# Performance work log

Hardware: AMD Instinct MI355X
Metric: run time of the kernel (lower is better)

## Reference

```python
import jax, jax.numpy as jnp
import numpy as np
import math

NB_HEADS = 16
NUM_BUCKETS = 32
MAX_DISTANCE = 128


def _rel_bucket(qlen, klen, num_buckets=NUM_BUCKETS, max_distance=MAX_DISTANCE):
    # static (numpy) computation of T5 relative-position buckets, bidirectional
    relpos = np.arange(qlen)[:, None] - np.arange(klen)[None, :]
    n = -relpos
    nb = num_buckets // 2
    ret = (n < 0).astype(np.int64) * nb
    n = np.abs(n)
    max_exact = nb // 2
    is_small = n < max_exact
    val_if_large = max_exact + (
        np.log(np.maximum(n, 1) / max_exact) / math.log(max_distance / max_exact) * (nb - max_exact)
    ).astype(np.int64)
    val_if_large = np.minimum(val_if_large, nb - 1)
    return ret + np.where(is_small, n, val_if_large)


def _layer_normalize(x):
    # faithful to source: mean/biased-std over last dim, NO epsilon, no affine
    m = jnp.mean(x, axis=-1, keepdims=True)
    var = jnp.mean((x - m) ** 2, axis=-1, keepdims=True)
    return (x - m) / jnp.sqrt(var)


def setup_inputs() -> dict:
    key = jax.random.key(0)
    ks = jax.random.split(key, 16)
    B, L, D, F = 4, 1024, 1024, 4096
    s = 0.02
    inp = {
        "x": jax.random.normal(ks[0], (B, L, D), jnp.float32),
        "padding_mask": jnp.ones((B, L), jnp.int32),
        "Wq": jax.random.normal(ks[1], (D, D), jnp.float32) * s,
        "bq": jnp.zeros((D,), jnp.float32),
        "Wk": jax.random.normal(ks[2], (D, D), jnp.float32) * s,
        "bk": jnp.zeros((D,), jnp.float32),
        "Wv": jax.random.normal(ks[3], (D, D), jnp.float32) * s,
        "bv": jnp.zeros((D,), jnp.float32),
        "Wo": jax.random.normal(ks[4], (D, D), jnp.float32) * s,
        "bo": jnp.zeros((D,), jnp.float32),
        "rel_emb": jax.random.normal(ks[5], (NUM_BUCKETS, NB_HEADS), jnp.float32) * s,
        "W1": jax.random.normal(ks[6], (F, D), jnp.float32) * s,
        "b1": jnp.zeros((F,), jnp.float32),
        "W2": jax.random.normal(ks[7], (D, F), jnp.float32) * s,
        "b2": jnp.zeros((D,), jnp.float32),
    }
    return inp


def reference(x, padding_mask, Wq, bq, Wk, bk, Wv, bv, Wo, bo, rel_emb, W1, b1, W2, b2):
    B, L, D = x.shape
    H = NB_HEADS
    dh = D // H

    q = x @ Wq.T + bq
    k = x @ Wk.T + bk
    v = x @ Wv.T + bv

    # NOTE: source does a RAW reshape (B, L, H*dh) -> (B*H, L, dh); reproduce exactly
    qm = q.reshape(B * H, L, dh)
    km = k.reshape(B * H, L, dh)
    vm = v.reshape(B * H, L, dh)

    scores = jnp.einsum("bqd,bkd->bqk", qm, km)  # (B*H, L, L), no 1/sqrt(dh) scaling in source

    # relative position bias: emb[bucket] -> (L, L, H), tile heads B times, permute
    buckets = jnp.asarray(_rel_bucket(L, L))
    pos = rel_emb[buckets]                      # (L, L, H)
    bias = jnp.transpose(jnp.tile(pos, (1, 1, B)), (2, 0, 1))  # (H*B, L, L)
    scores = scores + bias

    # padding mask in log space, tiled exactly like source's repeat+view
    pm = jnp.log(padding_mask.astype(jnp.float32))            # (B, L)
    mask = jnp.tile(pm[:, None, :], (1, L, H)).reshape(-1, L, L)  # (B*H, L, L)
    scores = scores + mask

    p = jax.nn.softmax(scores, axis=-1)  # dropout is identity at p=0 / eval
    att = (p @ vm).reshape(B, L, D)
    att = att @ Wo.T + bo

    att_out = _layer_normalize(att + x)
    ff = jax.nn.relu(att_out @ W1.T + b1) @ W2.T + b2
    ff_out = _layer_normalize(ff + att_out)
    return ff_out
```

## Files before the change

### kernel.cpp

```cpp
#include <hip/hip_runtime.h>
#include <hip/hip_bf16.h>

typedef __hip_bfloat16 bf16;
typedef __attribute__((ext_vector_type(8))) short s8v;
typedef __attribute__((ext_vector_type(4))) float f32x4;

__device__ __forceinline__ float bits2f(unsigned short u) {
    return __uint_as_float(((unsigned)u) << 16);
}
__device__ __forceinline__ unsigned short f2b(float f) {
    union { float f; unsigned u; } x{f};
    return (unsigned short)((x.u + 0x7fff + ((x.u >> 16) & 1)) >> 16);
}
__device__ __forceinline__ float to_f(float x) { return x; }
__device__ __forceinline__ float to_f(unsigned short x) { return bits2f(x); }

__device__ __forceinline__ void load4(const float* p, float* a) {
    float4 t = *(const float4*)p;
    a[0] = t.x; a[1] = t.y; a[2] = t.z; a[3] = t.w;
}
__device__ __forceinline__ void load4(const unsigned short* p, float* a) {
    ushort4 t = *(const ushort4*)p;
    a[0] = bits2f(t.x); a[1] = bits2f(t.y); a[2] = bits2f(t.z); a[3] = bits2f(t.w);
}

__global__ __launch_bounds__(256)
void cvt_all_kernel(const float* __restrict__ x,
                    const float* __restrict__ Wq, const float* __restrict__ Wk,
                    const float* __restrict__ Wv, const float* __restrict__ Wo,
                    const float* __restrict__ W1, const float* __restrict__ W2,
                    unsigned short* __restrict__ xb, unsigned short* __restrict__ Wqkvb,
                    unsigned short* __restrict__ Wob,
                    unsigned short* __restrict__ W1b, unsigned short* __restrict__ W2b)
{
    int i = blockIdx.x * 256 + threadIdx.x;
    const float* src; unsigned short* dst; int off;
    if (i < (1 << 20))      { src = x;  dst = xb;  off = i; }
    else if (i < (2 << 20)) { src = W1; dst = W1b; off = i - (1 << 20); }
    else if (i < (3 << 20)) { src = W2; dst = W2b; off = i - (2 << 20); }
    else {
        int j = i - (3 << 20);
        int sel = j >> 18;
        off = j & ((1 << 18) - 1);
        src = sel == 0 ? Wq : sel == 1 ? Wk : sel == 2 ? Wv : Wo;
        dst = sel == 3 ? Wob : Wqkvb + ((size_t)sel << 20);
    }
    float4 v = ((const float4*)src)[off];
    ushort4 o = { f2b(v.x), f2b(v.y), f2b(v.z), f2b(v.w) };
    ((ushort4*)dst)[off] = o;
}

__global__ void rbias_kernel(const float* __restrict__ rel_emb, unsigned short* __restrict__ rbias)
{
    int idx = blockIdx.x * 256 + threadIdx.x;
    if (idx >= 16 * 2048) return;
    int h = idx >> 11, q = idx & 2047;
    int n = q - 1023, ret = 0;
    if (n < 0) { ret = 16; n = -n; }
    int b;
    if (n < 8) b = n;
    else {
        double t = log((double)n / 8.0) / log(16.0) * 8.0;
        int v = 8 + (int)t;
        b = v < 15 ? v : 15;
    }
    rbias[idx] = f2b(rel_emb[(ret + b) * 16 + h]);
}

template<typename TC, typename TR, int RELU, int QKV>
__global__ __launch_bounds__(256)
void mfma_gemm(const unsigned short* __restrict__ A, int lda,
               const unsigned short* __restrict__ W, int ldw,
               const float* __restrict__ b0, const float* __restrict__ b1,
               const float* __restrict__ b2,
               const TR* __restrict__ res,
               void* __restrict__ C0, void* __restrict__ C1, void* __restrict__ C2,
               int ldc, int M, int N, int Ksplit)
{
    __shared__ unsigned short sm[2 * 128 * 32];
    unsigned short* As = sm;
    unsigned short* Ws = sm + 128 * 32;

    const int tid = threadIdx.x;
    const int w = tid >> 6, lane = tid & 63;
    const int quad = lane >> 4, col = lane & 15;
    const int m0 = blockIdx.y * 128, n0 = blockIdx.x * 128;
    const int wrow = (w & 1) * 64, wcol = (w >> 1) * 64;
    const int kz = blockIdx.z * Ksplit;

    const int srow   = lane >> 2;
    const int schunk = (lane & 3) ^ ((lane >> 4) & 3);

    f32x4 acc[4][4] = {};

    for (int k0 = kz; k0 < kz + Ksplit; k0 += 32) {
        __syncthreads();
        #pragma unroll
        for (int t = 0; t < 2; ++t) {
            const int rbase = w * 32 + t * 16;
            unsigned off = (unsigned)(rbase * 64);
            off = __builtin_amdgcn_readfirstlane(off);
            const unsigned short* ga = A + (size_t)(m0 + rbase + srow) * lda + k0 + schunk * 8;
            __builtin_amdgcn_global_load_lds(
                (const __attribute__((address_space(1))) unsigned int*)ga,
                (__attribute__((address_space(3))) unsigned int*)((char*)As + off), 16, 0, 0);
            const unsigned short* gw = W + (size_t)(n0 + rbase + srow) * ldw + k0 + schunk * 8;
            __builtin_amdgcn_global_load_lds(
                (const __attribute__((address_space(1))) unsigned int*)gw,
                (__attribute__((address_space(3))) unsigned int*)((char*)Ws + off), 16, 0, 0);
        }
        __syncthreads();

        s8v af[4], bfr[4];
        #pragma unroll
        for (int mt = 0; mt < 4; ++mt) {
            int rr = wrow + mt * 16 + col;
            af[mt] = *(const s8v*)(As + rr * 32 + ((quad ^ ((rr >> 2) & 3)) * 8));
        }
        #pragma unroll
        for (int nt = 0; nt < 4; ++nt) {
            int rr = wcol + nt * 16 + col;
            bfr[nt] = *(const s8v*)(Ws + rr * 32 + ((quad ^ ((rr >> 2) & 3)) * 8));
        }
        #pragma unroll
        for (int mt = 0; mt < 4; ++mt)
            #pragma unroll
            for (int nt = 0; nt < 4; ++nt)
                acc[mt][nt] = __builtin_amdgcn_mfma_f32_16x16x32_bf16(af[mt], bfr[nt], acc[mt][nt], 0, 0, 0);
    }

    if (QKV) {
        const int sel = n0 >> 10;
        unsigned short* Cb = (unsigned short*)(sel == 0 ? C0 : sel == 1 ? C1 : C2);
        const float* bs = sel == 0 ? b0 : sel == 1 ? b1 : b2;
        #pragma unroll
        for (int mt = 0; mt < 4; ++mt)
            #pragma unroll
            for (int rg = 0; rg < 4; ++rg) {
                int gm = m0 + wrow + mt * 16 + quad * 4 + rg;
                #pragma unroll
                for (int nt = 0; nt < 4; ++nt) {
                    int gnc = (n0 + wcol + nt * 16 + col) & 1023;
                    Cb[(size_t)gm * 1024 + gnc] = f2b(acc[mt][nt][rg] + bs[gnc]);
                }
            }
    } else {
        void* Cv = blockIdx.z ? C1 : C0;
        const bool z0 = (blockIdx.z == 0);
        #pragma unroll
        for (int mt = 0; mt < 4; ++mt)
            #pragma unroll
            for (int rg = 0; rg < 4; ++rg) {
                int gm = m0 + wrow + mt * 16 + quad * 4 + rg;
                #pragma unroll
                for (int nt = 0; nt < 4; ++nt) {
                    int gn = n0 + wcol + nt * 16 + col;
                    float c = acc[mt][nt][rg];
                    if (z0) {
                        if (b0)  c += b0[gn];
                        if (res) c += to_f(res[(size_t)gm * ldc + gn]);
                    }
                    if (RELU) c = fmaxf(c, 0.f);
                    if (sizeof(TC) == 2) ((unsigned short*)Cv)[(size_t)gm * ldc + gn] = f2b(c);
                    else                 ((float*)Cv)[(size_t)gm * ldc + gn] = c;
                }
            }
    }
}

__global__ __launch_bounds__(256)
void vtrans_kernel(const unsigned short* __restrict__ v, unsigned short* __restrict__ vt)
{
    __shared__ unsigned short t[64][68];
    const int bpmm = blockIdx.x;
    const int bp = bpmm >> 6, mm = bpmm & 63;
    const unsigned short* vr = v + (size_t)(bp * 64 + mm) * 1024;
    const int tid = threadIdx.x;
    #pragma unroll
    for (int it = 0; it < 4; ++it) {
        int c = (tid >> 6) + it * 4;
        int d = tid & 63;
        t[d][c] = vr[c * 64 + d];
    }
    __syncthreads();
    int d = tid >> 2, qq = tid & 3;
    ushort4 o = { t[d][qq * 4 + 0], t[d][qq * 4 + 1], t[d][qq * 4 + 2], t[d][qq * 4 + 3] };
    *(ushort4*)(vt + (size_t)bp * 65536 + (size_t)d * 1024 + mm * 16 + qq * 4) = o;
}

__global__ __launch_bounds__(256, 2)
void attn_mfma_kernel(const unsigned short* __restrict__ qb,
                      const unsigned short* __restrict__ kb,
                      const unsigned short* __restrict__ vt,
                      const unsigned short* __restrict__ rbias,
                      const int* __restrict__ pmask,
                      unsigned short* __restrict__ att)
{
    __shared__ unsigned short Qs[128 * 64];
    __shared__ unsigned short KP[128 * 64];
    __shared__ unsigned short Vt[64 * 128];
    __shared__ unsigned short rbs[2048];
    __shared__ unsigned short pmls[1024];

    const int tid = threadIdx.x;
    const int w = tid >> 6, lane = tid & 63;
    const int quad = lane >> 4, col = lane & 15;
    const int bp = blockIdx.x, i0 = blockIdx.y * 128;
    const int h = bp & 15, bb = bp >> 4;
    const size_t base = (size_t)bp << 16;
    const int myrow0 = w * 32, myrow1 = w * 32 + 16;

    {
        const unsigned short* qg = qb + base + (size_t)i0 * 64;
        #pragma unroll
        for (int it = 0; it < 4; ++it) {
            int idx = it * 256 + tid;
            int r = idx >> 3, c = idx & 7;
            s8v d = *(const s8v*)(qg + (size_t)r * 64 + (c ^ (r & 7)) * 8);
            *(s8v*)(Qs + r * 64 + c * 8) = d;
        }
    }
    {
        const unsigned short* rg = rbias + h * 2048;
        #pragma unroll
        for (int it = 0; it < 8; ++it) rbs[it * 256 + tid] = rg[it * 256 + tid];
    }
    #pragma unroll
    for (int it = 0; it < 4; ++it) {
        int j = it * 256 + tid;
        pmls[j] = f2b(__logf((float)pmask[bb * 1024 + j]));
    }

    f32x4 O0[4] = {}, O1[4] = {};
    float lrow0[4] = {0.f, 0.f, 0.f, 0.f};
    float lrow1[4] = {0.f, 0.f, 0.f, 0.f};

    unsigned short* Pw = KP + w * 2048;

    for (int jt = 0; jt < 8; ++jt) {
        const int j0 = jt * 128;
        __syncthreads();
        {
            const unsigned short* kg = kb + base + (size_t)j0 * 64;
            #pragma unroll
            for (int it = 0; it < 4; ++it) {
                int idx = it * 256 + tid;
                int r = idx >> 3, c = idx & 7;
                s8v d = *(const s8v*)(kg + (size_t)r * 64 + (c ^ (r & 7)) * 8);
                *(s8v*)(KP + r * 64 + c * 8) = d;
            }
            const unsigned short* vg = vt + base + j0;
            #pragma unroll
            for (int it = 0; it < 4; ++it) {
                int idx = it * 256 + tid;
                int r = idx >> 4, c = idx & 15;
                s8v d = *(const s8v*)(vg + (size_t)r * 1024 + (c ^ (r & 15)) * 8);
                *(s8v*)(Vt + r * 128 + c * 8) = d;
            }
        }
        __syncthreads();

        f32x4 S0[8] = {}, S1[8] = {};
        #pragma unroll
        for (int ks = 0; ks < 2; ++ks) {
            int ar0 = myrow0 + col, ar1 = myrow1 + col;
            s8v a0 = *(const s8v*)(Qs + ar0 * 64 + (((ks * 4 + quad) ^ (ar0 & 7)) * 8));
            s8v a1 = *(const s8v*)(Qs + ar1 * 64 + (((ks * 4 + quad) ^ (ar1 & 7)) * 8));
            #pragma unroll
            for (int ct = 0; ct < 8; ++ct) {
                int br = ct * 16 + col;
                s8v b = *(const s8v*)(KP + br * 64 + (((ks * 4 + quad) ^ (br & 7)) * 8));
                S0[ct] = __builtin_amdgcn_mfma_f32_16x16x32_bf16(a0, b, S0[ct], 0, 0, 0);
                S1[ct] = __builtin_amdgcn_mfma_f32_16x16x32_bf16(a1, b, S1[ct], 0, 0, 0);
            }
        }

        #pragma unroll
        for (int ct = 0; ct < 8; ++ct) {
            int gj = j0 + ct * 16 + col;
            float pmv = bits2f(pmls[gj]);
            int d0 = gj - (i0 + myrow0 + quad * 4) + 1023;
            int d1 = gj - (i0 + myrow1 + quad * 4) + 1023;
            #pragma unroll
            for (int r = 0; r < 4; ++r) {
                float e0 = __expf(S0[ct][r] + bits2f(rbs[d0 - r]) + pmv);
                float e1 = __expf(S1[ct][r] + bits2f(rbs[d1 - r]) + pmv);
                S0[ct][r] = e0; lrow0[r] += e0;
                S1[ct][r] = e1; lrow1[r] += e1;
            }
        }

        __syncthreads();

        #pragma unroll
        for (int ct = 0; ct < 8; ++ct)
            #pragma unroll
            for (int r = 0; r < 4; ++r) {
                int lr = quad * 4 + r;
                int j = ct * 16 + col;
                Pw[lr * 128 + (((j >> 3) ^ lr) << 3) + (j & 7)] = f2b(S0[ct][r]);
            }
        #pragma unroll
        for (int kt = 0; kt < 4; ++kt) {
            int pr = col;
            s8v a = *(const s8v*)(Pw + pr * 128 + (((kt * 4 + quad) ^ pr) * 8));
            #pragma unroll
            for (int nt = 0; nt < 4; ++nt) {
                int vr = nt * 16 + col;
                s8v b = *(const s8v*)(Vt + vr * 128 + (((kt * 4 + quad) ^ (vr & 15)) * 8));
                O0[nt] = __builtin_amdgcn_mfma_f32_16x16x32_bf16(a, b, O0[nt], 0, 0, 0);
            }
        }

        #pragma unroll
        for (int ct = 0; ct < 8; ++ct)
            #pragma unroll
            for (int r = 0; r < 4; ++r) {
                int lr = quad * 4 + r;
                int j = ct * 16 + col;
                Pw[lr * 128 + (((j >> 3) ^ lr) << 3) + (j & 7)] = f2b(S1[ct][r]);
            }
        #pragma unroll
        for (int kt = 0; kt < 4; ++kt) {
            int pr = col;
            s8v a = *(const s8v*)(Pw + pr * 128 + (((kt * 4 + quad) ^ pr) * 8));
            #pragma unroll
            for (int nt = 0; nt < 4; ++nt) {
                int vr = nt * 16 + col;
                s8v b = *(const s8v*)(Vt + vr * 128 + (((kt * 4 + quad) ^ (vr & 15)) * 8));
                O1[nt] = __builtin_amdgcn_mfma_f32_16x16x32_bf16(a, b, O1[nt], 0, 0, 0);
            }
        }
    }

    #pragma unroll
    for (int off = 1; off < 16; off <<= 1)
        #pragma unroll
        for (int r = 0; r < 4; ++r) {
            lrow0[r] += __shfl_xor(lrow0[r], off);
            lrow1[r] += __shfl_xor(lrow1[r], off);
        }
    #pragma unroll
    for (int r = 0; r < 4; ++r) {
        lrow0[r] = 1.f / lrow0[r];
        lrow1[r] = 1.f / lrow1[r];
    }

    unsigned short* ag0 = att + base + (size_t)(i0 + myrow0) * 64;
    unsigned short* ag1 = att + base + (size_t)(i0 + myrow1) * 64;
    #pragma unroll
    for (int nt = 0; nt < 4; ++nt)
        #pragma unroll
        for (int r = 0; r < 4; ++r) {
            ag0[(size_t)(quad * 4 + r) * 64 + nt * 16 + col] = f2b(O0[nt][r] * lrow0[r]);
            ag1[(size_t)(quad * 4 + r) * 64 + nt * 16 + col] = f2b(O1[nt][r] * lrow1[r]);
        }
}

template<typename TIN>
__global__ __launch_bounds__(256)
void ln_kernel(const TIN* __restrict__ in1, const TIN* __restrict__ in2,
               float* __restrict__ outF, unsigned short* __restrict__ outB)
{
    __shared__ float sred[8];
    const int row = blockIdx.x;
    const int tid = threadIdx.x;
    const size_t off = (size_t)row * 1024 + tid * 4;
    float a[4];
    load4(in1 + off, a);
    if (in2) {
        float b[4];
        load4(in2 + off, b);
        #pragma unroll
        for (int i = 0; i < 4; ++i) a[i] += b[i];
    }

    float lsum = a[0] + a[1] + a[2] + a[3];
    #pragma unroll
    for (int o = 32; o; o >>= 1) lsum += __shfl_down(lsum, o);
    const int lane = tid & 63, wid = tid >> 6;
    if (lane == 0) sred[wid] = lsum;
    __syncthreads();
    if (tid == 0) sred[4] = (sred[0] + sred[1] + sred[2] + sred[3]) * (1.f / 1024.f);
    __syncthreads();
    const float mean = sred[4];

    float d0 = a[0] - mean, d1 = a[1] - mean, d2 = a[2] - mean, d3 = a[3] - mean;
    float lsq = d0 * d0 + d1 * d1 + d2 * d2 + d3 * d3;
    #pragma unroll
    for (int o = 32; o; o >>= 1) lsq += __shfl_down(lsq, o);
    __syncthreads();
    if (lane == 0) sred[wid] = lsq;
    __syncthreads();
    if (tid == 0) sred[5] = rsqrtf((sred[0] + sred[1] + sred[2] + sred[3]) * (1.f / 1024.f));
    __syncthreads();
    const float r = sred[5];

    float o0 = d0 * r, o1 = d1 * r, o2 = d2 * r, o3 = d3 * r;
    if (outF) {
        float4 o = {o0, o1, o2, o3};
        *(float4*)&outF[off] = o;
    }
    if (outB) {
        ushort4 o = { f2b(o0), f2b(o1), f2b(o2), f2b(o3) };
        *(ushort4*)&outB[off] = o;
    }
}

extern "C" void kernel_launch(void* const* d_in, const int* in_sizes, int n_in,
                              void* d_out, int out_size, void* d_ws, size_t ws_size,
                              hipStream_t stream)
{
    const float* x     = (const float*)d_in[0];
    const int*   pmask = (const int*)  d_in[1];
    const float* Wq    = (const float*)d_in[2];
    const float* bq    = (const float*)d_in[3];
    const float* Wk    = (const float*)d_in[4];
    const float* bk    = (const float*)d_in[5];
    const float* Wv    = (const float*)d_in[6];
    const float* bv    = (const float*)d_in[7];
    const float* Wo    = (const float*)d_in[8];
    const float* bo    = (const float*)d_in[9];
    const float* rel   = (const float*)d_in[10];
    const float* W1    = (const float*)d_in[11];
    const float* b1    = (const float*)d_in[12];
    const float* W2    = (const float*)d_in[13];
    const float* b2    = (const float*)d_in[14];

    const int M = 4096, D = 1024;
    dim3 blk(256);

    char* ws = (char*)d_ws;
    unsigned short* W1b   = (unsigned short*)(ws);
    unsigned short* W2b   = (unsigned short*)(ws + ( 8u << 20));
    unsigned short* xb    = (unsigned short*)(ws + (16u << 20));
    unsigned short* Wqkvb = (unsigned short*)(ws + (24u << 20));
    unsigned short* Wob   = (unsigned short*)(ws + (30u << 20));
    unsigned short* qb    = (unsigned short*)(ws + (32u << 20));
    unsigned short* kb    = (unsigned short*)(ws + (40u << 20));
    unsigned short* vb    = (unsigned short*)(ws + (48u << 20));
    unsigned short* vt    = (unsigned short*)(ws + (56u << 20));
    unsigned short* rbias = (unsigned short*)(ws + (64u << 20));
    float*          tmpA    = (float*)(ws + (32u << 20));
    float*          tmpB    = (float*)(ws + (48u << 20));
    unsigned short* attoutB = (unsigned short*)(ws + (16u << 20));
    unsigned short* ff1     = (unsigned short*)(ws + (32u << 20));
    unsigned short* ff2a    = (unsigned short*)(ws);
    unsigned short* ff2b    = (unsigned short*)(ws + (24u << 20));
    unsigned short* attb    = (unsigned short*)d_out;

    cvt_all_kernel<<<16384, blk, 0, stream>>>(x, Wq, Wk, Wv, Wo, W1, W2,
                                              xb, Wqkvb, Wob, W1b, W2b);
    rbias_kernel<<<128, blk, 0, stream>>>(rel, rbias);

    mfma_gemm<unsigned short, float, 0, 1><<<dim3(24, 32), blk, 0, stream>>>(
        xb, D, Wqkvb, D, bq, bk, bv, (const float*)nullptr, qb, kb, vb, D, M, 3072, D);

    vtrans_kernel<<<4096, blk, 0, stream>>>(vb, vt);

    attn_mfma_kernel<<<dim3(64, 8), blk, 0, stream>>>(qb, kb, vt, rbias, pmask, attb);

    mfma_gemm<float, float, 0, 0><<<dim3(8, 32, 2), blk, 0, stream>>>(
        attb, D, Wob, D, bo, nullptr, nullptr, x, tmpA, tmpB, nullptr, D, M, D, 512);
    ln_kernel<float><<<4096, blk, 0, stream>>>(tmpA, tmpB, nullptr, attoutB);

    mfma_gemm<unsigned short, float, 1, 0><<<dim3(32, 32), blk, 0, stream>>>(
        attoutB, D, W1b, D, b1, nullptr, nullptr, (const float*)nullptr,
        ff1, nullptr, nullptr, 4096, M, 4096, D);
    mfma_gemm<unsigned short, unsigned short, 0, 0><<<dim3(8, 32, 2), blk, 0, stream>>>(
        ff1, 4096, W2b, 4096, b2, nullptr, nullptr, attoutB, ff2a, ff2b, nullptr, D, M, D, 2048);
    ln_kernel<unsigned short><<<4096, blk, 0, stream>>>(ff2a, ff2b, (float*)d_out, nullptr);
}
```

Measured before the change: 435.3 us.

## Add 256x256-tile 8-wave GEMM with direct-to-LDS loads for QKV and FFN

Adds a new bf16 GEMM kernel that uses 256x256 output tiles, 512 threads, double-buffered LDS filled by global_load_lds with an XOR swizzle, and a four-phase schedule that overlaps loads of the next K-slices with MFMA work. The QKV projection, FFN1 and FFN2 GEMMs switch to it, with a grid swizzle for L2 locality and fused bias, ReLU and residual epilogues. The goal is more data reuse per tile and better overlap of memory and MFMA than the old 128-tile kernel. The cost is 128KB of dynamic LDS per block and more complex synchronisation. The larger tiles also give fewer blocks, which may underfill the 256 CUs (192 for QKV, 256 for FFN1, 128 for FFN2).

New measurement: 463.1 us. 6.4% more time.

```diff
diff --git a/kernel.cpp b/kernel.cpp
--- a/kernel.cpp
+++ b/kernel.cpp
@@ -163,6 +163,179 @@
                     if (RELU) c = fmaxf(c, 0.f);
                     if (sizeof(TC) == 2) ((unsigned short*)Cv)[(size_t)gm * ldc + gn] = f2b(c);
                     else                 ((float*)Cv)[(size_t)gm * ldc + gn] = c;
+                }
+            }
+    }
+}
+
+
+#define SWZ(r) ((((r) >> 2) & 3) | ((((r) >> 2) & 1) << 2))
+
+__device__ __forceinline__ void stage_ht(const unsigned short* __restrict__ g, int ld,
+                                         int grow0, int kbase,
+                                         unsigned short* lds_half, int tid)
+{
+    #pragma unroll
+    for (int l = 0; l < 2; ++l) {
+        int idx = l * 512 + tid;
+        int r = idx >> 3;
+        int c = (idx & 7) ^ SWZ(r);
+        const unsigned short* src = g + (size_t)(grow0 + r) * ld + kbase + c * 8;
+        unsigned off = (unsigned)__builtin_amdgcn_readfirstlane((unsigned)((l * 512 + (tid & 448)) * 16));
+        __builtin_amdgcn_global_load_lds(
+            (const __attribute__((address_space(1))) unsigned int*)src,
+            (__attribute__((address_space(3))) unsigned int*)((char*)lds_half + off), 16, 0, 0);
+    }
+}
+
+#define PHASE(HM, HN, ...)                                                        \
+    {                                                                             \
+        __builtin_amdgcn_sched_barrier(0);                                        \
+        s8v a_[4][2], b_[2][2];                                                   \
+        _Pragma("unroll")                                                         \
+        for (int mt2 = 0; mt2 < 4; ++mt2) {                                       \
+            int r = ((HM) * 4 + mt2) * 32 + wm16 + col;                           \
+            _Pragma("unroll")                                                     \
+            for (int ks = 0; ks < 2; ++ks)                                        \
+                a_[mt2][ks] = *(const s8v*)(dA + r * 64 + (((ks * 4 + quad) ^ SWZ(r)) << 3)); \
+        }                                                                         \
+        _Pragma("unroll")                                                         \
+        for (int nt2 = 0; nt2 < 2; ++nt2) {                                       \
+            int r = ((HN) * 2 + nt2) * 64 + wn16 + col;                           \
+            _Pragma("unroll")                                                     \
+            for (int ks = 0; ks < 2; ++ks)                                        \
+                b_[nt2][ks] = *(const s8v*)(dB + r * 64 + (((ks * 4 + quad) ^ SWZ(r)) << 3)); \
+        }                                                                         \
+        __VA_ARGS__;                                                              \
+        __builtin_amdgcn_sched_barrier(0);                                        \
+        __builtin_amdgcn_s_barrier();                                             \
+        asm volatile("s_waitcnt lgkmcnt(0)" ::: "memory");                        \
+        __builtin_amdgcn_sched_barrier(0);                                        \
+        __builtin_amdgcn_s_setprio(1);                                            \
+        _Pragma("unroll")                                                         \
+        for (int ks = 0; ks < 2; ++ks)                                            \
+            _Pragma("unroll")                                                     \
+            for (int mt2 = 0; mt2 < 4; ++mt2)                                     \
+                _Pragma("unroll")                                                 \
+                for (int nt2 = 0; nt2 < 2; ++nt2)                                 \
+                    acc[(HM) * 4 + mt2][(HN) * 2 + nt2] =                         \
+                        __builtin_amdgcn_mfma_f32_16x16x32_bf16(                  \
+                            a_[mt2][ks], b_[nt2][ks], acc[(HM) * 4 + mt2][(HN) * 2 + nt2], 0, 0, 0); \
+        __builtin_amdgcn_s_setprio(0);                                            \
+        __builtin_amdgcn_sched_barrier(0);                                        \
+    }
+
+template<int MODE>
+__global__ __launch_bounds__(512, 2)
+void gemm256(const unsigned short* __restrict__ A, int lda,
+             const unsigned short* __restrict__ W, int ldw,
+             const float* __restrict__ bias0, const float* __restrict__ bias1,
+             const float* __restrict__ bias2,
+             const unsigned short* __restrict__ res,
+             unsigned short* __restrict__ C0, unsigned short* __restrict__ C1,
+             unsigned short* __restrict__ C2,
+             int NT, int Ksplit)
+{
+    extern __shared__ unsigned short sm[];
+    unsigned short* As0 = sm;
+    unsigned short* Bs0 = sm + 32768;
+
+    const int tid = threadIdx.x;
+    const int w = tid >> 6, lane = tid & 63;
+    const int quad = lane >> 4, col = lane & 15;
+    const int wm16 = (w & 1) * 16, wn16 = (w >> 1) * 16;
+
+    const int bid = blockIdx.x + gridDim.x * blockIdx.y;
+    const int nwg = gridDim.x * gridDim.y;
+    const int swz = (bid & 7) * (nwg >> 3) + (bid >> 3);
+    const int m0 = (swz / gridDim.x) * 256;
+    const int n0 = (swz % gridDim.x) * 256;
+    const int kz = blockIdx.z * Ksplit;
+
+    f32x4 acc[8][4] = {};
+
+    stage_ht(A, lda, m0,       kz,      As0,                tid);
+    stage_ht(W, ldw, n0,       kz,      Bs0,                tid);
+    stage_ht(A, lda, m0 + 128, kz,      As0 + 8192,         tid);
+    stage_ht(W, ldw, n0 + 128, kz,      Bs0 + 8192,         tid);
+    stage_ht(A, lda, m0,       kz + 64, As0 + 16384,        tid);
+    stage_ht(W, ldw, n0 + 128, kz + 64, Bs0 + 16384 + 8192, tid);
+    asm volatile("s_waitcnt vmcnt(4)" ::: "memory");
+    __builtin_amdgcn_sched_barrier(0);
+    __builtin_amdgcn_s_barrier();
+
+    for (int t = 0; t < NT; ++t) {
+        const int cur = t & 1;
+        const unsigned short* dA = As0 + cur * 16384;
+        const unsigned short* dB = Bs0 + cur * 16384;
+        unsigned short* Anx = As0 + (cur ^ 1) * 16384;
+        unsigned short* Bnx = Bs0 + (cur ^ 1) * 16384;
+        unsigned short* Acu = As0 + cur * 16384;
+        unsigned short* Bcu = Bs0 + cur * 16384;
+        const int k1 = kz + (t + 1) * 64, k2 = kz + (t + 2) * 64;
+        const bool s1 = (t + 1 < NT), s2 = (t + 2 < NT);
+
+        PHASE(0, 0, { if (s1) stage_ht(W, ldw, n0,       k1, Bnx,        tid); })
+        __builtin_amdgcn_s_barrier();
+        PHASE(0, 1, { if (s1) stage_ht(A, lda, m0 + 128, k1, Anx + 8192, tid); })
+        __builtin_amdgcn_s_barrier();
+        PHASE(1, 1, { if (s2) stage_ht(A, lda, m0,       k2, Acu,        tid); })
+        __builtin_amdgcn_s_barrier();
+        PHASE(1, 0, { if (s2) stage_ht(W, ldw, n0 + 128, k2, Bcu + 8192, tid); })
+        if (s2) { asm volatile("s_waitcnt vmcnt(4)" ::: "memory"); }
+        else    { asm volatile("s_waitcnt vmcnt(0)" ::: "memory"); }
+        __builtin_amdgcn_sched_barrier(0);
+        __builtin_amdgcn_s_barrier();
+    }
+
+    const int rb = m0 + wm16 + quad * 4;
+    const int cb = wn16 + col;
+    if (MODE == 0) {
+        const int sel = n0 >> 10;
+        unsigned short* Cb = sel == 0 ? C0 : sel == 1 ? C1 : C2;
+        const float* bs = sel == 0 ? bias0 : sel == 1 ? bias1 : bias2;
+        const int nb = (n0 & 1023) + cb;
+        float bv[4];
+        #pragma unroll
+        for (int nt = 0; nt < 4; ++nt) bv[nt] = bs[nb + nt * 64];
+        #pragma unroll
+        for (int mt = 0; mt < 8; ++mt)
+            #pragma unroll
+            for (int rg = 0; rg < 4; ++rg) {
+                const size_t ro = (size_t)(rb + mt * 32 + rg) * 1024 + nb;
+                #pragma unroll
+                for (int nt = 0; nt < 4; ++nt)
+                    Cb[ro + nt * 64] = f2b(acc[mt][nt][rg] + bv[nt]);
+            }
+    } else if (MODE == 1) {
+        float bv[4];
+        #pragma unroll
+        for (int nt = 0; nt < 4; ++nt) bv[nt] = bias0[n0 + cb + nt * 64];
+        #pragma unroll
+        for (int mt = 0; mt < 8; ++mt)
+            #pragma unroll
+            for (int rg = 0; rg < 4; ++rg) {
+                const size_t ro = (size_t)(rb + mt * 32 + rg) * 4096 + n0 + cb;
+                #pragma unroll
+                for (int nt = 0; nt < 4; ++nt)
+                    C0[ro + nt * 64] = f2b(fmaxf(acc[mt][nt][rg] + bv[nt], 0.f));
+            }
+    } else {
+        unsigned short* Cb = blockIdx.z ? C1 : C0;
+        const bool z0 = (blockIdx.z == 0);
+        float bv[4];
+        #pragma unroll
+        for (int nt = 0; nt < 4; ++nt) bv[nt] = z0 ? bias0[n0 + cb + nt * 64] : 0.f;
+        #pragma unroll
+        for (int mt = 0; mt < 8; ++mt)
+            #pragma unroll
+            for (int rg = 0; rg < 4; ++rg) {
+                const size_t ro = (size_t)(rb + mt * 32 + rg) * 1024 + n0 + cb;
+                #pragma unroll
+                for (int nt = 0; nt < 4; ++nt) {
+                    float c = acc[mt][nt][rg] + bv[nt];
+                    if (z0) c += bits2f(res[ro + nt * 64]);
+                    Cb[ro + nt * 64] = f2b(c);
                 }
             }
     }
@@ -449,12 +622,23 @@
     unsigned short* ff2b    = (unsigned short*)(ws + (24u << 20));
     unsigned short* attb    = (unsigned short*)d_out;
 
+    static bool attrset = false;
+    if (!attrset) {
+        hipFuncSetAttribute(reinterpret_cast<const void*>(gemm256<0>),
+                            hipFuncAttributeMaxDynamicSharedMemorySize, 131072);
+        hipFuncSetAttribute(reinterpret_cast<const void*>(gemm256<1>),
+                            hipFuncAttributeMaxDynamicSharedMemorySize, 131072);
+        hipFuncSetAttribute(reinterpret_cast<const void*>(gemm256<2>),
+                            hipFuncAttributeMaxDynamicSharedMemorySize, 131072);
+        attrset = true;
+    }
+
     cvt_all_kernel<<<16384, blk, 0, stream>>>(x, Wq, Wk, Wv, Wo, W1, W2,
                                               xb, Wqkvb, Wob, W1b, W2b);
     rbias_kernel<<<128, blk, 0, stream>>>(rel, rbias);
 
-    mfma_gemm<unsigned short, float, 0, 1><<<dim3(24, 32), blk, 0, stream>>>(
-        xb, D, Wqkvb, D, bq, bk, bv, (const float*)nullptr, qb, kb, vb, D, M, 3072, D);
+    gemm256<0><<<dim3(12, 16), dim3(512), 131072, stream>>>(
+        xb, D, Wqkvb, D, bq, bk, bv, nullptr, qb, kb, vb, 16, 0);
 
     vtrans_kernel<<<4096, blk, 0, stream>>>(vb, vt);
 
@@ -464,10 +648,9 @@
         attb, D, Wob, D, bo, nullptr, nullptr, x, tmpA, tmpB, nullptr, D, M, D, 512);
     ln_kernel<float><<<4096, blk, 0, stream>>>(tmpA, tmpB, nullptr, attoutB);
 
-    mfma_gemm<unsigned short, float, 1, 0><<<dim3(32, 32), blk, 0, stream>>>(
-        attoutB, D, W1b, D, b1, nullptr, nullptr, (const float*)nullptr,
-        ff1, nullptr, nullptr, 4096, M, 4096, D);
-    mfma_gemm<unsigned short, unsigned short, 0, 0><<<dim3(8, 32, 2), blk, 0, stream>>>(
-        ff1, 4096, W2b, 4096, b2, nullptr, nullptr, attoutB, ff2a, ff2b, nullptr, D, M, D, 2048);
+    gemm256<1><<<dim3(16, 16), dim3(512), 131072, stream>>>(
+        attoutB, D, W1b, D, b1, nullptr, nullptr, nullptr, ff1, nullptr, nullptr, 16, 0);
+    gemm256<2><<<dim3(4, 16, 2), dim3(512), 131072, stream>>>(
+        ff1, 4096, W2b, 4096, b2, nullptr, nullptr, attoutB, ff2a, ff2b, nullptr, 32, 2048);
     ln_kernel<unsigned short><<<4096, blk, 0, stream>>>(ff2a, ff2b, (float*)d_out, nullptr);
 }
```
